# Performance work log

Measured on AMD Instinct MI355X. Metric: run time of the kernel, lower is better.

## Reference

```python
import jax, jax.numpy as jnp
import numpy as np

B = 1024
IN_SIZ = 16384
OUT_SIZ = 16384
C = 8          # channel_siz
NLVL = 10
IFS = IN_SIZ // 2 ** NLVL                                   # 16, in_filter_siz
KLVL = min(int(np.floor(np.log2(OUT_SIZ / 2))), NLVL)       # 10
OFS = OUT_SIZ // 2 ** KLVL                                  # 16, out_filter_siz
STD = 0.9


def setup_inputs() -> dict:
    key = jax.random.key(0)
    ks = jax.random.split(key, 2 * NLVL + 3)
    inp = {}
    inp["x"] = jax.random.normal(ks[0], (B, IN_SIZ, 1), jnp.float32)
    inp["in_filter"] = jax.random.normal(ks[1], (IFS, 1, C), jnp.float32) * STD
    inp["in_bias"] = jnp.zeros((C,), jnp.float32)
    for lvl in range(1, NLVL + 1):
        k = 2 ** lvl
        inp[f"W{lvl}"] = jax.random.normal(ks[2 * lvl], (k, 2, C, C), jnp.float32) * STD
        inp[f"b{lvl}"] = jnp.zeros((k, C), jnp.float32)
    inp["fea_dense"] = jax.random.normal(ks[-1], (2 ** KLVL, C, OFS), jnp.float32) * STD
    return inp


def _level(v, W, b):
    # v: [Kp, B, L, C] parent branches; W: [2*Kp, 2, C, C]; b: [2*Kp, C]
    # kernel-2 stride-2 conv1d: out[t] = relu(x[2t] @ W[0] + x[2t+1] @ W[1] + b)
    Kp, Bn, L, Cc = v.shape
    xp = v.reshape(Kp, Bn, L // 2, 2, Cc)
    xr = jnp.repeat(xp, 2, axis=0)  # child itk reads parent itk // 2
    y = jnp.einsum('kbtsc,kscd->kbtd', xr, W) + b[:, None, None, :]
    return jax.nn.relu(y)


def reference(x, in_filter, in_bias,
              W1, b1, W2, b2, W3, b3, W4, b4, W5, b5,
              W6, b6, W7, b7, W8, b8, W9, b9, W10, b10,
              fea_dense):
    Ws = [W1, W2, W3, W4, W5, W6, W7, W8, W9, W10]
    bs = [b1, b2, b3, b4, b5, b6, b7, b8, b9, b10]
    Bn = x.shape[0]
    # input conv1d: kernel=IFS, stride=IFS (non-overlapping) == blocked matmul
    xin = x[..., 0].reshape(Bn, 2 ** NLVL, IFS)                       # [B, 1024, 16]
    v = jax.nn.relu(jnp.einsum('bnf,fc->bnc', xin, in_filter[:, 0, :]) + in_bias)
    v = v[None]                                                        # [1, B, 1024, C]
    for lvl in range(NLVL):  # klvl == nlvl: all levels branch (tree doubling)
        v = _level(v, Ws[lvl], bs[lvl])
    # v: [2^klvl, B, 1, C] -> per-branch dense feature map
    out = jnp.einsum('kbc,kcf->bkf', v[:, :, 0, :], fea_dense)         # [B, 1024, OFS]
    return out.reshape(Bn, OUT_SIZ, 1)
```

## Files before the change

### kernel.cpp

```cpp
#include <hip/hip_runtime.h>

struct PrepPtrs {
  const float* W[7]; const float* Bv[7]; const float* F; const float* fb;
  const float* W8; const float* B8; const float* W9; const float* B9;
  const float* W10; const float* B10;
};

__device__ __forceinline__ int cz(int c) { return c ^ ((c >> 3) & 3); }

__device__ __forceinline__ float4 relu4(float4 a) {
  return make_float4(fmaxf(a.x,0.f), fmaxf(a.y,0.f), fmaxf(a.z,0.f), fmaxf(a.w,0.f));
}
__device__ __forceinline__ void fma4(float4& acc, float s, const float4& wv) {
  acc.x = fmaf(s, wv.x, acc.x); acc.y = fmaf(s, wv.y, acc.y);
  acc.z = fmaf(s, wv.z, acc.z); acc.w = fmaf(s, wv.w, acc.w);
}
__device__ __forceinline__ float4 add4(float4 a, float4 b) {
  return make_float4(a.x+b.x, a.y+b.y, a.z+b.z, a.w+b.w);
}

__device__ __forceinline__ float4 entApply(const float4* __restrict__ e4,
                                           float4 A0, float4 A1,
                                           float4 C0, float4 C1) {
  float4 a0 = e4[16];
  float4 a1 = make_float4(0.f, 0.f, 0.f, 0.f);
  float4 a2 = make_float4(0.f, 0.f, 0.f, 0.f);
  float4 a3 = make_float4(0.f, 0.f, 0.f, 0.f);
  fma4(a0, A0.x, e4[0]);  fma4(a1, A0.y, e4[1]);  fma4(a2, A0.z, e4[2]);  fma4(a3, A0.w, e4[3]);
  fma4(a0, A1.x, e4[4]);  fma4(a1, A1.y, e4[5]);  fma4(a2, A1.z, e4[6]);  fma4(a3, A1.w, e4[7]);
  fma4(a0, C0.x, e4[8]);  fma4(a1, C0.y, e4[9]);  fma4(a2, C0.z, e4[10]); fma4(a3, C0.w, e4[11]);
  fma4(a0, C1.x, e4[12]); fma4(a1, C1.y, e4[13]); fma4(a2, C1.z, e4[14]); fma4(a3, C1.w, e4[15]);
  return relu4(add4(add4(a0, a1), add4(a2, a3)));
}

__global__ void bfly_prep(PrepPtrs P, float* __restrict__ wt) {
  int e = blockIdx.x * 256 + threadIdx.x;
  if (e >= 4094 * 68) return;
  int ent = e / 68, r = e % 68, dd = r & 3;
  const float* Ws; const float* Bs; int th;
  if (ent < 62) {
    if (ent < 60) {
      int lvl, base;
      if (ent < 4)       { lvl = 1; base = 0;  }
      else if (ent < 12) { lvl = 2; base = 4;  }
      else if (ent < 28) { lvl = 3; base = 12; }
      else               { lvl = 4; base = 28; }
      int k = (ent - base) >> 1; th = ent & 1;
      Ws = P.W[lvl-1] + k*128; Bs = P.Bv[lvl-1] + k*8;
    } else {
      th = ent - 60; Ws = P.F; Bs = P.fb;
    }
  } else if (ent < 510) {
    int eb = ent - 62;
    int q = eb / 56, rem = eb % 56;
    int lvl, Kl, base;
    if (rem < 8)       { lvl = 5; Kl = 4;  base = 0;  }
    else if (rem < 24) { lvl = 6; Kl = 8;  base = 8;  }
    else               { lvl = 7; Kl = 16; base = 24; }
    int rr = rem - base; int lk = rr >> 1; th = rr & 1;
    int kg = q * Kl + lk;
    Ws = P.W[lvl-1] + kg*128; Bs = P.Bv[lvl-1] + kg*8;
  } else if (ent < 1022) {
    int ec = ent - 510; int k = ec >> 1; th = ec & 1;
    Ws = P.W8 + k*128; Bs = P.B8 + k*8;
  } else if (ent < 2046) {
    int ec = ent - 1022; int k = ec >> 1; th = ec & 1;
    Ws = P.W9 + k*128; Bs = P.B9 + k*8;
  } else {
    int ec = ent - 2046; int k = ec >> 1; th = ec & 1;
    Ws = P.W10 + k*128; Bs = P.B10 + k*8;
  }
  float v;
  if (r < 64) { int s = r >> 5, c = (r >> 2) & 7; v = Ws[s*64 + c*8 + th*4 + dd]; }
  else v = Bs[th*4 + dd];
  wt[ent * 80 + r] = v;
}

template<int L>
__device__ __forceinline__ void ka_level2(const float4* __restrict__ src,
                                          float4* __restrict__ dst,
                                          const float4* __restrict__ wt4,
                                          int lane, int w) {
  constexpr int Tc = 1024 >> L;
  constexpr int entBase = ((1 << L) - 2) * 2;
  constexpr int TB = 1 << (4 - L);
  const int kp = w >> (4 - L);
  const int tb = w & (TB - 1);
  const int t = lane + tb * 64;
  const int pb = kp * (2 * Tc) + 2 * t;
  const int cb = cz(pb);
  const int cb1 = cb ^ 1;
  float4 A0 = src[cb],        C0 = src[cb1];
  float4 A1 = src[cb + 1024], C1 = src[cb1 + 1024];
  float4* pD = dst + cz(2 * kp * Tc + t);
#pragma unroll
  for (int kk = 0; kk < 2; ++kk)
#pragma unroll
    for (int th = 0; th < 2; ++th) {
      const float4* e4 = wt4 + (entBase + (2 * kp + kk) * 2 + th) * 20;
      pD[kk * Tc + th * 1024] = entApply(e4, A0, A1, C0, C1);
    }
}

__global__ __launch_bounds__(512, 2) void bfly_ka(
    const float* __restrict__ x, const float* __restrict__ wt,
    float* __restrict__ st1)
{
  __shared__ float4 sA[2048], sB[2048];
  const int tid = threadIdx.x, b = blockIdx.x;
  const int lane = tid & 63;
  const int w = __builtin_amdgcn_readfirstlane(tid >> 6);
  const int th = w & 1, wq = w >> 1;
  const float4* wt4 = (const float4*)wt;

  {
    const float4* e4 = wt4 + (60 + th) * 20;
    const float* xb = x + (size_t)b * 16384;
#pragma unroll
    for (int i = 0; i < 4; ++i) {
      int n = lane + wq * 64 + i * 256;
      const float4* xr = (const float4*)(xb + n * 16);
      float4 x0 = xr[0], x1 = xr[1], x2 = xr[2], x3 = xr[3];
      sA[cz(th * 1024 + n)] = entApply(e4, x0, x1, x2, x3);
    }
  }
  __syncthreads();
  ka_level2<1>(sA, sB, wt4, lane, w); __syncthreads();
  ka_level2<2>(sB, sA, wt4, lane, w); __syncthreads();
  ka_level2<3>(sA, sB, wt4, lane, w); __syncthreads();
  ka_level2<4>(sB, sA, wt4, lane, w); __syncthreads();

  float4* o4 = (float4*)st1;
#pragma unroll
  for (int it = 0; it < 4; ++it) {
    int o = tid + it * 512;
    int t4 = o & 63, k4 = (o >> 6) & 15, h = o >> 10;
    o4[((size_t)(h * 16 + k4) * 1024 + b) * 64 + t4] = sA[cz(o)];
  }
}

template<int LV>
__device__ __forceinline__ void kb_level2(float4* __restrict__ s,
                                          const float4* __restrict__ wb4,
                                          int lane, int w) {
  constexpr int Tc = 1 << (10 - LV);
  constexpr int entB = (LV == 5) ? 0 : (LV == 6) ? 8 : 24;
  int kp, bl, t;
  if constexpr (LV == 5)      { kp = w >> 2; bl = ((w & 3) << 1) | (lane >> 5); t = lane & 31; }
  else if constexpr (LV == 6) { kp = w >> 1; bl = ((w & 1) << 2) | (lane >> 4); t = lane & 15; }
  else                        { kp = w;      bl = lane >> 3;                    t = lane & 7;  }
  const int pb = bl * 256 + kp * (2 * Tc) + 2 * t;
  const int cb = cz(pb);
  const int cb1 = cb ^ 1;
  float4 A0 = s[cb],       C0 = s[cb1];
  float4 A1 = s[cb + 128], C1 = s[cb1 + 128];
#pragma unroll
  for (int kk = 0; kk < 2; ++kk) {
    float4* pD = s + cz(bl * 256 + (2 * kp + kk) * Tc + t);
#pragma unroll
    for (int th = 0; th < 2; ++th) {
      const float4* e4 = wb4 + (entB + (2 * kp + kk) * 2 + th) * 20;
      pD[th * 128] = entApply(e4, A0, A1, C0, C1);
    }
  }
}

__global__ __launch_bounds__(512, 3) void bfly_kb(
    const float* __restrict__ st1, const float* __restrict__ wt,
    float* __restrict__ st2)
{
  __shared__ float4 s0[2048];
  const int tid = threadIdx.x;
  const int q = blockIdx.x, bt = blockIdx.y;
  const int lane = tid & 63;
  const int w = __builtin_amdgcn_readfirstlane(tid >> 6);
  const float4* wb4 = (const float4*)wt + 1240 + q * 56 * 20;
  const float4* i4 = (const float4*)st1;

#pragma unroll
  for (int it = 0; it < 4; ++it) {
    int o = tid + it * 512;
    int t4 = o & 63, lk4 = (o >> 6) & 1, h = (o >> 7) & 1, bl = o >> 8;
    float4 v = i4[((size_t)(h * 16 + 2 * q + lk4) * 1024 + bt * 8 + bl) * 64 + t4];
    s0[cz(bl * 256 + h * 128 + lk4 * 64 + t4)] = v;
  }
  __syncthreads();
  kb_level2<5>(s0, wb4, lane, w); __syncthreads();
  kb_level2<6>(s0, wb4, lane, w); __syncthreads();
  kb_level2<7>(s0, wb4, lane, w); __syncthreads();

  float4* o4 = (float4*)st2;
#pragma unroll
  for (int it = 0; it < 4; ++it) {
    int o = tid + it * 512;
    int bl = o & 7, t7 = (o >> 3) & 7, h = (o >> 6) & 1, lk7 = o >> 7;
    float4 v = s0[cz(bl * 256 + h * 128 + lk7 * 8 + t7)];
    o4[((size_t)((16 * q + lk7) * 8 + t7) * 2 + h) * 1024 + bt * 8 + bl] = v;
  }
}

__global__ __launch_bounds__(512, 2) void bfly_kc(
    const float* __restrict__ st, const float* __restrict__ wt,
    const float* __restrict__ fea, float* __restrict__ out)
{
  __shared__ float4 sA[1024], sB[1024];
  const int tid = threadIdx.x;
  const int j = blockIdx.x, b0 = blockIdx.y * 64;
  const int bb = tid & 63;
  const int w = __builtin_amdgcn_readfirstlane(tid >> 6);
  const float4* wt4 = (const float4*)wt;

  {
    const float4* s4 = (const float4*)st;
#pragma unroll
    for (int it = 0; it < 2; ++it) {
      int idx = tid + it * 512;
      int bl = idx & 63, h = (idx >> 6) & 1, t = idx >> 7;
      sA[h * 512 + t * 64 + bl] = s4[((size_t)((j * 8 + t) * 2 + h)) * 1024 + b0 + bl];
    }
  }
  __syncthreads();

#pragma unroll
  for (int ii = 0; ii < 2; ++ii) {
    int s = w + ii * 8;
    int th = s >> 3, k = (s >> 2) & 1, t = s & 3;
    const float4* e4 = wt4 + (510 + (2 * j + k) * 2 + th) * 20;
    float4 A0 = sA[(2*t) * 64 + bb],   A1 = sA[512 + (2*t) * 64 + bb];
    float4 C0 = sA[(2*t+1) * 64 + bb], C1 = sA[512 + (2*t+1) * 64 + bb];
    sB[th * 512 + (2*t + k) * 64 + bb] = entApply(e4, A0, A1, C0, C1);
  }
  __syncthreads();
#pragma unroll
  for (int ii = 0; ii < 2; ++ii) {
    int s = w + ii * 8;
    int th = s >> 3, k9 = (s >> 1) & 3, t9 = s & 1;
    const float4* e4 = wt4 + (1022 + (4 * j + k9) * 2 + th) * 20;
    int p0 = 4 * t9 + (k9 >> 1), p1 = p0 + 2;
    float4 A0 = sB[p0 * 64 + bb], A1 = sB[512 + p0 * 64 + bb];
    float4 C0 = sB[p1 * 64 + bb], C1 = sB[512 + p1 * 64 + bb];
    sA[th * 512 + (t9 * 4 + k9) * 64 + bb] = entApply(e4, A0, A1, C0, C1);
  }
  __syncthreads();
#pragma unroll
  for (int ii = 0; ii < 2; ++ii) {
    int s = w + ii * 8;
    int th = s >> 3, k10 = s & 7;
    const float4* e4 = wt4 + (2046 + (8 * j + k10) * 2 + th) * 20;
    int p0 = k10 >> 1, p1 = p0 + 4;
    float4 A0 = sA[p0 * 64 + bb], A1 = sA[512 + p0 * 64 + bb];
    float4 C0 = sA[p1 * 64 + bb], C1 = sA[512 + p1 * 64 + bb];
    sB[th * 512 + k10 * 64 + bb] = entApply(e4, A0, A1, C0, C1);
  }
  __syncthreads();
  {
    int cc = tid & 31, bgrp = tid >> 5;
    int k = cc >> 2, fq = cc & 3;
    const float* fp = fea + (size_t)(j * 8 + k) * 128 + fq * 4;
    float4 f0 = *(const float4*)(fp);        float4 f1 = *(const float4*)(fp + 16);
    float4 f2 = *(const float4*)(fp + 32);   float4 f3 = *(const float4*)(fp + 48);
    float4 f4_ = *(const float4*)(fp + 64);  float4 f5 = *(const float4*)(fp + 80);
    float4 f6 = *(const float4*)(fp + 96);   float4 f7 = *(const float4*)(fp + 112);
#pragma unroll
    for (int it = 0; it < 4; ++it) {
      int b_l = bgrp + it * 16;
      float4 s0v = sB[k * 64 + b_l];
      float4 s1v = sB[512 + k * 64 + b_l];
      float4 a0 = make_float4(0.f,0.f,0.f,0.f), a1 = make_float4(0.f,0.f,0.f,0.f);
      float4 a2 = make_float4(0.f,0.f,0.f,0.f), a3 = make_float4(0.f,0.f,0.f,0.f);
      fma4(a0, s0v.x, f0);  fma4(a1, s0v.y, f1);
      fma4(a2, s0v.z, f2);  fma4(a3, s0v.w, f3);
      fma4(a0, s1v.x, f4_); fma4(a1, s1v.y, f5);
      fma4(a2, s1v.z, f6);  fma4(a3, s1v.w, f7);
      float4 acc = add4(add4(a0, a1), add4(a2, a3));
      *(float4*)(out + ((size_t)(b0 + b_l)) * 16384 + j * 128 + k * 16 + fq * 4) = acc;
    }
  }
}

extern "C" void kernel_launch(void* const* d_in, const int* in_sizes, int n_in,
                              void* d_out, int out_size, void* d_ws, size_t ws_size,
                              hipStream_t stream) {
  const float* x  = (const float*)d_in[0];
  PrepPtrs P;
  P.F  = (const float*)d_in[1];
  P.fb = (const float*)d_in[2];
  for (int l = 0; l < 7; ++l) {
    P.W[l]  = (const float*)d_in[3 + 2 * l];
    P.Bv[l] = (const float*)d_in[4 + 2 * l];
  }
  P.W8  = (const float*)d_in[17];
  P.B8  = (const float*)d_in[18];
  P.W9  = (const float*)d_in[19];
  P.B9  = (const float*)d_in[20];
  P.W10 = (const float*)d_in[21];
  P.B10 = (const float*)d_in[22];
  const float* fea = (const float*)d_in[23];
  float* wt  = (float*)d_ws;
  float* st2 = (float*)d_ws + 393216;
  float* st1 = (float*)d_out;
  float* out = (float*)d_out;

  bfly_prep<<<dim3(1088), dim3(256), 0, stream>>>(P, wt);
  bfly_ka<<<dim3(1024), dim3(512), 0, stream>>>(x, wt, st1);
  bfly_kb<<<dim3(8, 128), dim3(512), 0, stream>>>(st1, wt, st2);
  bfly_kc<<<dim3(128, 16), dim3(512), 0, stream>>>(st2, wt, fea, out);
}
```

Baseline: 100.5 us.

## Split first butterfly kernel across two blocks per batch row

```diff
diff --git a/kernel.cpp b/kernel.cpp
--- a/kernel.cpp
+++ b/kernel.cpp
@@ -77,37 +77,67 @@
 }
 
 template<int L>
-__device__ __forceinline__ void ka_level2(const float4* __restrict__ src,
+__device__ __forceinline__ void ka_level3(const float4* __restrict__ src,
                                           float4* __restrict__ dst,
                                           const float4* __restrict__ wt4,
                                           int lane, int w) {
-  constexpr int Tc = 1024 >> L;
+  constexpr int T = 512 >> L;
   constexpr int entBase = ((1 << L) - 2) * 2;
-  constexpr int TB = 1 << (4 - L);
-  const int kp = w >> (4 - L);
-  const int tb = w & (TB - 1);
-  const int t = lane + tb * 64;
-  const int pb = kp * (2 * Tc) + 2 * t;
-  const int cb = cz(pb);
-  const int cb1 = cb ^ 1;
-  float4 A0 = src[cb],        C0 = src[cb1];
-  float4 A1 = src[cb + 1024], C1 = src[cb1 + 1024];
-  float4* pD = dst + cz(2 * kp * Tc + t);
-#pragma unroll
-  for (int kk = 0; kk < 2; ++kk)
-#pragma unroll
-    for (int th = 0; th < 2; ++th) {
-      const float4* e4 = wt4 + (entBase + (2 * kp + kk) * 2 + th) * 20;
-      pD[kk * Tc + th * 1024] = entApply(e4, A0, A1, C0, C1);
-    }
-}
-
-__global__ __launch_bounds__(512, 2) void bfly_ka(
+  const int th = w & 1, wq = w >> 1;
+  if constexpr (L == 1) {
+#pragma unroll
+    for (int it = 0; it < 2; ++it) {
+      const int k = wq & 1;
+      const int t = lane + (wq >> 1) * 64 + it * 128;
+      const float4* e4 = wt4 + (entBase + k * 2 + th) * 20;
+      int pb = (k >> 1) * (2 * T) + 2 * t;
+      int cb = cz(pb), cb1 = cb ^ 1;
+      float4 A0 = src[cb], C0 = src[cb1], A1 = src[cb + 512], C1 = src[cb1 + 512];
+      dst[cz(th * 512 + k * T + t)] = entApply(e4, A0, A1, C0, C1);
+    }
+  } else if constexpr (L == 2) {
+#pragma unroll
+    for (int it = 0; it < 2; ++it) {
+      const int k = wq;
+      const int t = lane + it * 64;
+      const float4* e4 = wt4 + (entBase + k * 2 + th) * 20;
+      int pb = (k >> 1) * (2 * T) + 2 * t;
+      int cb = cz(pb), cb1 = cb ^ 1;
+      float4 A0 = src[cb], C0 = src[cb1], A1 = src[cb + 512], C1 = src[cb1 + 512];
+      dst[cz(th * 512 + k * T + t)] = entApply(e4, A0, A1, C0, C1);
+    }
+  } else if constexpr (L == 3) {
+#pragma unroll
+    for (int ik = 0; ik < 2; ++ik) {
+      const int k = wq + 4 * ik;
+      const int t = lane;
+      const float4* e4 = wt4 + (entBase + k * 2 + th) * 20;
+      int pb = (k >> 1) * (2 * T) + 2 * t;
+      int cb = cz(pb), cb1 = cb ^ 1;
+      float4 A0 = src[cb], C0 = src[cb1], A1 = src[cb + 512], C1 = src[cb1 + 512];
+      dst[cz(th * 512 + k * T + t)] = entApply(e4, A0, A1, C0, C1);
+    }
+  } else {
+#pragma unroll
+    for (int ik = 0; ik < 4; ++ik) {
+      const int k = wq + 4 * ik;
+      const int t = lane & 31;
+      const float4* e4 = wt4 + (entBase + k * 2 + th) * 20;
+      int pb = (k >> 1) * (2 * T) + 2 * t;
+      int cb = cz(pb), cb1 = cb ^ 1;
+      float4 A0 = src[cb], C0 = src[cb1], A1 = src[cb + 512], C1 = src[cb1 + 512];
+      dst[cz(th * 512 + k * T + t)] = entApply(e4, A0, A1, C0, C1);
+    }
+  }
+}
+
+__global__ __launch_bounds__(512, 3) void bfly_ka(
     const float* __restrict__ x, const float* __restrict__ wt,
     float* __restrict__ st1)
 {
-  __shared__ float4 sA[2048], sB[2048];
-  const int tid = threadIdx.x, b = blockIdx.x;
+  __shared__ float4 sA[1024], sB[1024];
+  const int tid = threadIdx.x;
+  const int b = blockIdx.x >> 1, half = blockIdx.x & 1;
   const int lane = tid & 63;
   const int w = __builtin_amdgcn_readfirstlane(tid >> 6);
   const int th = w & 1, wq = w >> 1;
@@ -115,27 +145,28 @@
 
   {
     const float4* e4 = wt4 + (60 + th) * 20;
-    const float* xb = x + (size_t)b * 16384;
-#pragma unroll
-    for (int i = 0; i < 4; ++i) {
+    const float* xb = x + (size_t)b * 16384 + half * 8192;
+#pragma unroll
+    for (int i = 0; i < 2; ++i) {
       int n = lane + wq * 64 + i * 256;
       const float4* xr = (const float4*)(xb + n * 16);
       float4 x0 = xr[0], x1 = xr[1], x2 = xr[2], x3 = xr[3];
-      sA[cz(th * 1024 + n)] = entApply(e4, x0, x1, x2, x3);
-    }
-  }
-  __syncthreads();
-  ka_level2<1>(sA, sB, wt4, lane, w); __syncthreads();
-  ka_level2<2>(sB, sA, wt4, lane, w); __syncthreads();
-  ka_level2<3>(sA, sB, wt4, lane, w); __syncthreads();
-  ka_level2<4>(sB, sA, wt4, lane, w); __syncthreads();
+      sA[cz(th * 512 + n)] = entApply(e4, x0, x1, x2, x3);
+    }
+  }
+  __syncthreads();
+  ka_level3<1>(sA, sB, wt4, lane, w); __syncthreads();
+  ka_level3<2>(sB, sA, wt4, lane, w); __syncthreads();
+  ka_level3<3>(sA, sB, wt4, lane, w); __syncthreads();
+  ka_level3<4>(sB, sA, wt4, lane, w); __syncthreads();
 
   float4* o4 = (float4*)st1;
 #pragma unroll
-  for (int it = 0; it < 4; ++it) {
+  for (int it = 0; it < 2; ++it) {
     int o = tid + it * 512;
-    int t4 = o & 63, k4 = (o >> 6) & 15, h = o >> 10;
-    o4[((size_t)(h * 16 + k4) * 1024 + b) * 64 + t4] = sA[cz(o)];
+    int t4l = o & 31, k4 = (o >> 5) & 15, h = o >> 9;
+    float4 v = sA[cz(h * 512 + k4 * 32 + t4l)];
+    o4[((size_t)(h * 16 + k4) * 1024 + b) * 64 + half * 32 + t4l] = v;
   }
 }
 
@@ -302,7 +333,7 @@
   float* out = (float*)d_out;
 
   bfly_prep<<<dim3(1088), dim3(256), 0, stream>>>(P, wt);
-  bfly_ka<<<dim3(1024), dim3(512), 0, stream>>>(x, wt, st1);
+  bfly_ka<<<dim3(2048), dim3(512), 0, stream>>>(x, wt, st1);
   bfly_kb<<<dim3(8, 128), dim3(512), 0, stream>>>(st1, wt, st2);
   bfly_kc<<<dim3(128, 16), dim3(512), 0, stream>>>(st2, wt, fea, out);
 }
```

Measured after the change: 93.07 us. 1.08x faster.

## Make first-stage butterfly in-place with bit-reversed layout and split batches across blocks

Applied to the files above, without the earlier changes.

```diff
diff --git a/kernel.cpp b/kernel.cpp
--- a/kernel.cpp
+++ b/kernel.cpp
@@ -77,65 +77,79 @@
 }
 
 template<int L>
-__device__ __forceinline__ void ka_level2(const float4* __restrict__ src,
-                                          float4* __restrict__ dst,
-                                          const float4* __restrict__ wt4,
-                                          int lane, int w) {
-  constexpr int Tc = 1024 >> L;
+__device__ __forceinline__ void ka_inplace(float4* __restrict__ s,
+                                           const float4* __restrict__ wt4,
+                                           int lane, int w) {
   constexpr int entBase = ((1 << L) - 2) * 2;
-  constexpr int TB = 1 << (4 - L);
-  const int kp = w >> (4 - L);
-  const int tb = w & (TB - 1);
-  const int t = lane + tb * 64;
-  const int pb = kp * (2 * Tc) + 2 * t;
-  const int cb = cz(pb);
-  const int cb1 = cb ^ 1;
-  float4 A0 = src[cb],        C0 = src[cb1];
-  float4 A1 = src[cb + 1024], C1 = src[cb1 + 1024];
-  float4* pD = dst + cz(2 * kp * Tc + t);
-#pragma unroll
-  for (int kk = 0; kk < 2; ++kk)
-#pragma unroll
-    for (int th = 0; th < 2; ++th) {
-      const float4* e4 = wt4 + (entBase + (2 * kp + kk) * 2 + th) * 20;
-      pD[kk * Tc + th * 1024] = entApply(e4, A0, A1, C0, C1);
-    }
-}
-
-__global__ __launch_bounds__(512, 2) void bfly_ka(
+  constexpr int CL = 1 << (L - 1);
+  const int c = w & (CL - 1);
+  const int tpart = w >> (L - 1);
+  const int bb = lane >> 5, ul5 = lane & 31;
+  const int t = ul5 + tpart * 32;
+  int kp;
+  if constexpr (L == 1)      kp = 0;
+  else if constexpr (L == 2) kp = c;
+  else if constexpr (L == 3) kp = ((c & 1) << 1) | (c >> 1);
+  else                       kp = ((c & 1) << 2) | (c & 2) | (c >> 2);
+  const int s0 = (t << L) + c;
+  const int s1 = s0 + CL;
+  const int cb0 = cz(bb * 512 + s0);
+  const int cb1 = cz(bb * 512 + s1);
+  float4 A0 = s[cb0], A1 = s[cb0 + 1024];
+  float4 C0 = s[cb1], C1 = s[cb1 + 1024];
+  const float4* e00 = wt4 + (entBase + (2 * kp) * 2 + 0) * 20;
+  const float4* e01 = wt4 + (entBase + (2 * kp) * 2 + 1) * 20;
+  const float4* e10 = wt4 + (entBase + (2 * kp + 1) * 2 + 0) * 20;
+  const float4* e11 = wt4 + (entBase + (2 * kp + 1) * 2 + 1) * 20;
+  float4 o00 = entApply(e00, A0, A1, C0, C1);
+  float4 o01 = entApply(e01, A0, A1, C0, C1);
+  float4 o10 = entApply(e10, A0, A1, C0, C1);
+  float4 o11 = entApply(e11, A0, A1, C0, C1);
+  s[cb0] = o00; s[cb0 + 1024] = o01;
+  s[cb1] = o10; s[cb1 + 1024] = o11;
+}
+
+__global__ __launch_bounds__(512, 4) void bfly_ka(
     const float* __restrict__ x, const float* __restrict__ wt,
     float* __restrict__ st1)
 {
-  __shared__ float4 sA[2048], sB[2048];
-  const int tid = threadIdx.x, b = blockIdx.x;
+  __shared__ float4 s[2048];
+  const int tid = threadIdx.x;
+  const int bp = blockIdx.x >> 1, half = blockIdx.x & 1;
   const int lane = tid & 63;
   const int w = __builtin_amdgcn_readfirstlane(tid >> 6);
-  const int th = w & 1, wq = w >> 1;
+  const int bb = lane >> 5, ul5 = lane & 31;
   const float4* wt4 = (const float4*)wt;
 
   {
-    const float4* e4 = wt4 + (60 + th) * 20;
-    const float* xb = x + (size_t)b * 16384;
-#pragma unroll
-    for (int i = 0; i < 4; ++i) {
-      int n = lane + wq * 64 + i * 256;
+    const float4* e0 = wt4 + 60 * 20;
+    const float4* e1 = wt4 + 61 * 20;
+    const float* xb = x + (size_t)(2 * bp + bb) * 16384 + half * 8192;
+#pragma unroll
+    for (int it = 0; it < 2; ++it) {
+      int n = ul5 + w * 32 + it * 256;
       const float4* xr = (const float4*)(xb + n * 16);
       float4 x0 = xr[0], x1 = xr[1], x2 = xr[2], x3 = xr[3];
-      sA[cz(th * 1024 + n)] = entApply(e4, x0, x1, x2, x3);
-    }
-  }
-  __syncthreads();
-  ka_level2<1>(sA, sB, wt4, lane, w); __syncthreads();
-  ka_level2<2>(sB, sA, wt4, lane, w); __syncthreads();
-  ka_level2<3>(sA, sB, wt4, lane, w); __syncthreads();
-  ka_level2<4>(sB, sA, wt4, lane, w); __syncthreads();
+      int cb = cz(bb * 512 + n);
+      s[cb]        = entApply(e0, x0, x1, x2, x3);
+      s[cb + 1024] = entApply(e1, x0, x1, x2, x3);
+    }
+  }
+  __syncthreads();
+  ka_inplace<1>(s, wt4, lane, w); __syncthreads();
+  ka_inplace<2>(s, wt4, lane, w); __syncthreads();
+  ka_inplace<3>(s, wt4, lane, w); __syncthreads();
+  ka_inplace<4>(s, wt4, lane, w); __syncthreads();
 
   float4* o4 = (float4*)st1;
 #pragma unroll
   for (int it = 0; it < 4; ++it) {
-    int o = tid + it * 512;
-    int t4 = o & 63, k4 = (o >> 6) & 15, h = o >> 10;
-    o4[((size_t)(h * 16 + k4) * 1024 + b) * 64 + t4] = sA[cz(o)];
+    int combo = it * 8 + w;
+    int h = combo >> 4, k4 = combo & 15;
+    int br4 = ((k4 & 1) << 3) | ((k4 & 2) << 1) | ((k4 & 4) >> 1) | ((k4 & 8) >> 3);
+    int t4 = ul5;
+    float4 v = s[cz(bb * 512 + t4 * 16 + br4) + h * 1024];
+    o4[((size_t)(h * 16 + k4) * 1024 + (2 * bp + bb)) * 64 + half * 32 + t4] = v;
   }
 }
 
@@ -165,7 +179,7 @@
   }
 }
 
-__global__ __launch_bounds__(512, 3) void bfly_kb(
+__global__ __launch_bounds__(512, 4) void bfly_kb(
     const float* __restrict__ st1, const float* __restrict__ wt,
     float* __restrict__ st2)
 {
@@ -199,7 +213,7 @@
   }
 }
 
-__global__ __launch_bounds__(512, 2) void bfly_kc(
+__global__ __launch_bounds__(512, 3) void bfly_kc(
     const float* __restrict__ st, const float* __restrict__ wt,
     const float* __restrict__ fea, float* __restrict__ out)
 {
```

Result: no change. 100.4 us (-0.2%).

## Compute first butterfly levels in registers per thread, move level 4 to kb

Applied to the files above, without the earlier changes.

```diff
diff --git a/kernel.cpp b/kernel.cpp
--- a/kernel.cpp
+++ b/kernel.cpp
@@ -76,67 +76,64 @@
   wt[ent * 80 + r] = v;
 }
 
-template<int L>
-__device__ __forceinline__ void ka_level2(const float4* __restrict__ src,
-                                          float4* __restrict__ dst,
-                                          const float4* __restrict__ wt4,
-                                          int lane, int w) {
-  constexpr int Tc = 1024 >> L;
-  constexpr int entBase = ((1 << L) - 2) * 2;
-  constexpr int TB = 1 << (4 - L);
-  const int kp = w >> (4 - L);
-  const int tb = w & (TB - 1);
-  const int t = lane + tb * 64;
-  const int pb = kp * (2 * Tc) + 2 * t;
-  const int cb = cz(pb);
-  const int cb1 = cb ^ 1;
-  float4 A0 = src[cb],        C0 = src[cb1];
-  float4 A1 = src[cb + 1024], C1 = src[cb1 + 1024];
-  float4* pD = dst + cz(2 * kp * Tc + t);
-#pragma unroll
-  for (int kk = 0; kk < 2; ++kk)
-#pragma unroll
-    for (int th = 0; th < 2; ++th) {
-      const float4* e4 = wt4 + (entBase + (2 * kp + kk) * 2 + th) * 20;
-      pD[kk * Tc + th * 1024] = entApply(e4, A0, A1, C0, C1);
-    }
-}
-
-__global__ __launch_bounds__(512, 2) void bfly_ka(
+__global__ __launch_bounds__(256, 2) void bfly_ka(
     const float* __restrict__ x, const float* __restrict__ wt,
     float* __restrict__ st1)
 {
-  __shared__ float4 sA[2048], sB[2048];
-  const int tid = threadIdx.x, b = blockIdx.x;
-  const int lane = tid & 63;
-  const int w = __builtin_amdgcn_readfirstlane(tid >> 6);
-  const int th = w & 1, wq = w >> 1;
+  const int tid = threadIdx.x;
+  const int T = tid & 127;
+  const int bb = tid >> 7;
+  const int b = blockIdx.x * 2 + bb;
   const float4* wt4 = (const float4*)wt;
-
-  {
+  const float4* xb4 = (const float4*)x + (size_t)b * 4096 + T * 32;
+
+  float4 s[16], n[16];
+
+#pragma unroll
+  for (int th = 0; th < 2; ++th) {
     const float4* e4 = wt4 + (60 + th) * 20;
-    const float* xb = x + (size_t)b * 16384;
-#pragma unroll
-    for (int i = 0; i < 4; ++i) {
-      int n = lane + wq * 64 + i * 256;
-      const float4* xr = (const float4*)(xb + n * 16);
-      float4 x0 = xr[0], x1 = xr[1], x2 = xr[2], x3 = xr[3];
-      sA[cz(th * 1024 + n)] = entApply(e4, x0, x1, x2, x3);
-    }
-  }
-  __syncthreads();
-  ka_level2<1>(sA, sB, wt4, lane, w); __syncthreads();
-  ka_level2<2>(sB, sA, wt4, lane, w); __syncthreads();
-  ka_level2<3>(sA, sB, wt4, lane, w); __syncthreads();
-  ka_level2<4>(sB, sA, wt4, lane, w); __syncthreads();
-
+#pragma unroll
+    for (int r = 0; r < 8; ++r) {
+      float4 x0 = xb4[r*4], x1 = xb4[r*4+1], x2 = xb4[r*4+2], x3 = xb4[r*4+3];
+      s[r*2+th] = entApply(e4, x0, x1, x2, x3);
+    }
+  }
+#pragma unroll
+  for (int th = 0; th < 2; ++th)
+#pragma unroll
+    for (int k = 0; k < 2; ++k) {
+      const float4* e4 = wt4 + (0 + k*2 + th) * 20;
+#pragma unroll
+      for (int t = 0; t < 4; ++t)
+        n[(k*4+t)*2+th] = entApply(e4, s[(2*t)*2], s[(2*t)*2+1],
+                                       s[(2*t+1)*2], s[(2*t+1)*2+1]);
+    }
+#pragma unroll
+  for (int th = 0; th < 2; ++th)
+#pragma unroll
+    for (int k = 0; k < 4; ++k) {
+      const float4* e4 = wt4 + (4 + k*2 + th) * 20;
+      const int kp = k >> 1;
+#pragma unroll
+      for (int t = 0; t < 2; ++t)
+        s[(k*2+t)*2+th] = entApply(e4, n[(kp*4+2*t)*2], n[(kp*4+2*t)*2+1],
+                                       n[(kp*4+2*t+1)*2], n[(kp*4+2*t+1)*2+1]);
+    }
+#pragma unroll
+  for (int th = 0; th < 2; ++th)
+#pragma unroll
+    for (int k = 0; k < 8; ++k) {
+      const float4* e4 = wt4 + (12 + k*2 + th) * 20;
+      const int kp = k >> 1;
+      n[k*2+th] = entApply(e4, s[(kp*2)*2], s[(kp*2)*2+1],
+                               s[(kp*2+1)*2], s[(kp*2+1)*2+1]);
+    }
   float4* o4 = (float4*)st1;
 #pragma unroll
-  for (int it = 0; it < 4; ++it) {
-    int o = tid + it * 512;
-    int t4 = o & 63, k4 = (o >> 6) & 15, h = o >> 10;
-    o4[((size_t)(h * 16 + k4) * 1024 + b) * 64 + t4] = sA[cz(o)];
-  }
+  for (int k = 0; k < 8; ++k)
+#pragma unroll
+    for (int th = 0; th < 2; ++th)
+      o4[((size_t)(k*2+th) * 1024 + b) * 128 + T] = n[k*2+th];
 }
 
 template<int LV>
@@ -174,15 +171,33 @@
   const int q = blockIdx.x, bt = blockIdx.y;
   const int lane = tid & 63;
   const int w = __builtin_amdgcn_readfirstlane(tid >> 6);
-  const float4* wb4 = (const float4*)wt + 1240 + q * 56 * 20;
+  const float4* wt4 = (const float4*)wt;
+  const float4* wb4 = wt4 + 1240 + q * 56 * 20;
   const float4* i4 = (const float4*)st1;
 
 #pragma unroll
   for (int it = 0; it < 4; ++it) {
     int o = tid + it * 512;
-    int t4 = o & 63, lk4 = (o >> 6) & 1, h = (o >> 7) & 1, bl = o >> 8;
-    float4 v = i4[((size_t)(h * 16 + 2 * q + lk4) * 1024 + bt * 8 + bl) * 64 + t4];
-    s0[cz(bl * 256 + h * 128 + lk4 * 64 + t4)] = v;
+    int t3 = o & 127, h = (o >> 7) & 1, bl = o >> 8;
+    float4 v = i4[((size_t)(q * 2 + h) * 1024 + bt * 8 + bl) * 128 + t3];
+    s0[cz(bl * 256 + h * 128 + t3)] = v;
+  }
+  __syncthreads();
+  {
+    const float4* eb = wt4 + (28 + 4 * q) * 20;
+    int bl = w, t = lane;
+    int pb = bl * 256 + 2 * t;
+    int cb = cz(pb), cb1 = cb ^ 1;
+    float4 A0 = s0[cb], C0 = s0[cb1], A1 = s0[cb + 128], C1 = s0[cb1 + 128];
+#pragma unroll
+    for (int kk = 0; kk < 2; ++kk) {
+      float4* pD = s0 + cz(bl * 256 + kk * 64 + t);
+#pragma unroll
+      for (int th = 0; th < 2; ++th) {
+        const float4* e4 = eb + (kk * 2 + th) * 20;
+        pD[th * 128] = entApply(e4, A0, A1, C0, C1);
+      }
+    }
   }
   __syncthreads();
   kb_level2<5>(s0, wb4, lane, w); __syncthreads();
@@ -302,7 +317,7 @@
   float* out = (float*)d_out;
 
   bfly_prep<<<dim3(1088), dim3(256), 0, stream>>>(P, wt);
-  bfly_ka<<<dim3(1024), dim3(512), 0, stream>>>(x, wt, st1);
+  bfly_ka<<<dim3(512), dim3(256), 0, stream>>>(x, wt, st1);
   bfly_kb<<<dim3(8, 128), dim3(512), 0, stream>>>(st1, wt, st2);
   bfly_kc<<<dim3(128, 16), dim3(512), 0, stream>>>(st2, wt, fea, out);
 }
```

Result: no change. 101.3 us (+0.7%).
